# Optimization experiments

Hardware: AMD Instinct MI355X
Metric: run time of the kernel (lower is better)

## Reference

```python
import jax, jax.numpy as jnp
import numpy as np
from jax import lax

DN = ('NCHW', 'OIHW', 'NCHW')
NUM_HEADS = 6


def _conv1x1(x, w):
    return lax.conv_general_dilated(x, w, (1, 1), 'VALID', dimension_numbers=DN)


def _dwconv3x3(x, w):
    # depthwise 3x3, groups == channels, padding 1
    return lax.conv_general_dilated(x, w, (1, 1), ((1, 1), (1, 1)),
                                    dimension_numbers=DN,
                                    feature_group_count=w.shape[0])


def setup_inputs() -> dict:
    key = jax.random.key(0)
    ks = jax.random.split(key, 7)
    b, dim, h, w = 4, 192, 128, 128
    inp = {
        'x': jax.random.normal(ks[0], (b, dim, h, w), jnp.float32),
        'ref': jax.random.normal(ks[1], (b, dim, h, w), jnp.float32),
        'w_qkv': jax.random.normal(ks[2], (dim * 3, dim, 1, 1), jnp.float32) * 0.05,
        'w_dw': jax.random.normal(ks[3], (dim * 3, 1, 3, 3), jnp.float32) * 0.1,
        'w_proj': jax.random.normal(ks[4], (dim, dim, 1, 1), jnp.float32) * 0.05,
        'temperature': jnp.ones((NUM_HEADS, 1, 1), jnp.float32),
        'attn_w': 0.2 * jnp.ones((4,), jnp.float32),
    }
    return inp


def reference(x, ref, w_qkv, w_dw, w_proj, temperature, attn_w):
    b, c, h, w = x.shape
    heads = NUM_HEADS
    C = c // heads  # per-head channel dim
    hw = h * w

    qkv = _dwconv3x3(_conv1x1(x, w_qkv), w_dw)        # [b, 3c, h, w]
    ref_qkv = _dwconv3x3(_conv1x1(ref, w_qkv), w_dw)  # shared weights

    q_shared = qkv[:, :c]            # q from x
    k_shared = ref_qkv[:, c:2 * c]   # k from ref
    v_shared = ref_qkv[:, 2 * c:]    # v from ref

    def to_heads(t):  # [b, c, h, w] -> [b, head, C, hw]
        return t.reshape(b, heads, C, hw)

    q = to_heads(q_shared)
    k = to_heads(k_shared)
    v = to_heads(v_shared)

    # L2-normalize along token dim (last axis)
    q = q / jnp.maximum(jnp.linalg.norm(q, axis=-1, keepdims=True), 1e-12)
    k = k / jnp.maximum(jnp.linalg.norm(k, axis=-1, keepdims=True), 1e-12)

    # channel-wise attention: [b, head, C, C]
    attn = jnp.einsum('bhcn,bhdn->bhcd', q, k) * temperature

    ks_list = [int(C / 2), int(C * 2 / 3), int(C * 3 / 4), int(C * 4 / 5)]
    neg_inf = jnp.asarray(-jnp.inf, attn.dtype)

    out = 0.0
    for i, ki in enumerate(ks_list):
        vals = lax.top_k(attn, ki)[0]            # [b, head, C, ki]
        thr = vals[..., -1:]                     # k-th largest per row
        a = jnp.where(attn >= thr, attn, neg_inf)
        a = jax.nn.softmax(a, axis=-1)
        out = out + attn_w[i] * jnp.einsum('bhcd,bhdn->bhcn', a, v)

    out = out.reshape(b, c, h, w)
    return _conv1x1(out, w_proj)
```

## Files before the change

kernel.cpp:

```cpp
#include <hip/hip_runtime.h>
#include <cstdint>
#include <cstddef>

typedef unsigned short u16;
typedef unsigned int u32;
typedef __attribute__((ext_vector_type(2))) float f32x2;
typedef __attribute__((ext_vector_type(4))) float f32x4;
typedef __attribute__((ext_vector_type(8))) short short8;
typedef __attribute__((ext_vector_type(2))) u32 u32x2;
typedef __attribute__((ext_vector_type(4))) u32 u32x4;

#define DEV static __device__ __forceinline__
#define HW 16384

DEV u16 f2bf(float f) {
  u32 u = __float_as_uint(f);
  u = (u + 0x7fffu + ((u >> 16) & 1u)) >> 16;
  return (u16)u;
}
DEV float bf2f(u16 h) { return __uint_as_float(((u32)h) << 16); }

DEV u32 packsplit(float f) {
  u16 h = f2bf(f);
  u16 l = f2bf(f - bf2f(h));
  return (u32)h | ((u32)l << 16);
}
DEV void unpack8(const u32* w, short8& hi, short8& lo) {
  #pragma unroll
  for (int i = 0; i < 8; ++i) {
    hi[i] = (short)(u16)w[i];
    lo[i] = (short)(u16)(w[i] >> 16);
  }
}
DEV void mfma3(f32x4& acc, short8 ah, short8 al, short8 bh, short8 bl) {
  acc = __builtin_amdgcn_mfma_f32_16x16x32_bf16(ah, bh, acc, 0, 0, 0);
  acc = __builtin_amdgcn_mfma_f32_16x16x32_bf16(ah, bl, acc, 0, 0, 0);
  acc = __builtin_amdgcn_mfma_f32_16x16x32_bf16(al, bh, acc, 0, 0, 0);
}

__global__ __launch_bounds__(256) void ksplit(const float* __restrict__ in,
                                              u32* __restrict__ out, int n) {
  int i = blockIdx.x * 256 + threadIdx.x;
  if (i < n) out[i] = packsplit(in[i]);
}

template<int ABATCH, int BPACKED>
__global__ __launch_bounds__(512, 4) void gemm2(const u32* __restrict__ Asp,
                                                const u32* __restrict__ B,
                                                float* __restrict__ C) {
  __shared__ u32 As[192 * 34];
  __shared__ u32 Bs[64 * 34];
  const int t = threadIdx.x, lane = t & 63, wid = t >> 6;
  const int b = blockIdx.z, n0 = blockIdx.x * 64;
  const u32* Ab = ABATCH ? (Asp + (size_t)b * 192 * 192) : Asp;
  const u32* Bb = B + (size_t)b * 192 * (size_t)HW;
  float* Cb = C + (size_t)b * 192 * (size_t)HW;
  const int wr = wid >> 2, wc = wid & 3;
  const int g = lane >> 4, r16 = lane & 15;
  const int b_n = (t & 15) * 4, b_k = t >> 4;
  f32x4 acc[6] = {};

  u32x4 Breg, Bnext;
  u32x4 Areg[3];
  Breg = *(const u32x4*)&Bb[(size_t)b_k * HW + n0 + b_n];
  #pragma unroll
  for (int i = 0; i < 3; ++i) {
    int vi = t + i * 512;
    Areg[i] = *(const u32x4*)&Ab[(size_t)(vi >> 3) * 192 + ((vi & 7) << 2)];
  }
  #pragma unroll 1
  for (int p = 0; p < 6; ++p) {
    #pragma unroll
    for (int j = 0; j < 4; ++j)
      Bs[(b_n + j) * 34 + b_k] = BPACKED ? Breg[j] : packsplit(__uint_as_float(Breg[j]));
    #pragma unroll
    for (int i = 0; i < 3; ++i) {
      int vi = t + i * 512;
      int row = vi >> 3, kc = (vi & 7) << 2;
      u32x2 v0 = {Areg[i][0], Areg[i][1]};
      u32x2 v1 = {Areg[i][2], Areg[i][3]};
      *(u32x2*)&As[row * 34 + kc] = v0;
      *(u32x2*)&As[row * 34 + kc + 2] = v1;
    }
    if (p < 5)
      Bnext = *(const u32x4*)&Bb[(size_t)((p + 1) * 32 + b_k) * HW + n0 + b_n];
    __syncthreads();
    if (p < 5) {
      #pragma unroll
      for (int i = 0; i < 3; ++i) {
        int vi = t + i * 512;
        Areg[i] = *(const u32x4*)&Ab[(size_t)(vi >> 3) * 192 + (p + 1) * 32 + ((vi & 7) << 2)];
      }
    }
    u32 bw[8];
    {
      const u32* bp = &Bs[(wc * 16 + r16) * 34 + g * 8];
      *(u32x2*)&bw[0] = *(const u32x2*)&bp[0];
      *(u32x2*)&bw[2] = *(const u32x2*)&bp[2];
      *(u32x2*)&bw[4] = *(const u32x2*)&bp[4];
      *(u32x2*)&bw[6] = *(const u32x2*)&bp[6];
    }
    short8 bh, bl; unpack8(bw, bh, bl);
    #pragma unroll
    for (int mf = 0; mf < 6; ++mf) {
      u32 aw[8];
      const u32* ap = &As[(wr * 96 + mf * 16 + r16) * 34 + g * 8];
      *(u32x2*)&aw[0] = *(const u32x2*)&ap[0];
      *(u32x2*)&aw[2] = *(const u32x2*)&ap[2];
      *(u32x2*)&aw[4] = *(const u32x2*)&ap[4];
      *(u32x2*)&aw[6] = *(const u32x2*)&ap[6];
      short8 ah, al; unpack8(aw, ah, al);
      acc[mf] = __builtin_amdgcn_mfma_f32_16x16x32_bf16(ah, bh, acc[mf], 0, 0, 0);
      acc[mf] = __builtin_amdgcn_mfma_f32_16x16x32_bf16(ah, bl, acc[mf], 0, 0, 0);
      acc[mf] = __builtin_amdgcn_mfma_f32_16x16x32_bf16(al, bh, acc[mf], 0, 0, 0);
    }
    __syncthreads();
    Breg = Bnext;
  }
  #pragma unroll
  for (int mf = 0; mf < 6; ++mf)
    #pragma unroll
    for (int rr = 0; rr < 4; ++rr)
      Cb[(size_t)(wr * 96 + mf * 16 + g * 4 + rr) * HW + n0 + wc * 16 + r16] =
          acc[mf][rr];
}

template<int SSQ>
__global__ __launch_bounds__(512) void k2_dw(const float* __restrict__ Tin,
                                             const float* __restrict__ wdw, int wco,
                                             u32* __restrict__ O,
                                             float* __restrict__ ssq, int sspath) {
  const int rt = blockIdx.x, cg = blockIdx.y, b = blockIdx.z;
  const int t = threadIdx.x, lane = t & 63, w = t >> 6;
  __shared__ float In[8][10][132];
  for (int idx = t; idx < 10400; idx += 512) {
    int ch = idx / 1300, rem = idx % 1300;
    int r = rem / 130, ci = rem % 130;
    int gr = rt * 8 + r - 1, gc = ci - 1;
    float v = 0.f;
    if (gr >= 0 && gr < 128 && gc >= 0 && gc < 128)
      v = Tin[((size_t)b * 192 + cg * 8 + ch) * HW + gr * 128 + gc];
    In[ch][r][ci] = v;
  }
  float wv[9];
  #pragma unroll
  for (int j = 0; j < 9; ++j) wv[j] = wdw[(size_t)(wco + cg * 8 + w) * 9 + j];
  __syncthreads();
  float s = 0.f;
  u32* Op = O + ((size_t)b * 192 + cg * 8 + w) * HW + rt * 8 * 128 + 2 * lane;
  #pragma unroll
  for (int i = 0; i < 8; ++i) {
    float a0 = 0.f, a1 = 0.f;
    #pragma unroll
    for (int dr = 0; dr < 3; ++dr) {
      f32x2 u0 = *(const f32x2*)&In[w][i + dr][2 * lane];
      f32x2 u1 = *(const f32x2*)&In[w][i + dr][2 * lane + 2];
      a0 += wv[dr * 3] * u0[0] + wv[dr * 3 + 1] * u0[1] + wv[dr * 3 + 2] * u1[0];
      a1 += wv[dr * 3] * u0[1] + wv[dr * 3 + 1] * u1[0] + wv[dr * 3 + 2] * u1[1];
    }
    u32x2 o = {packsplit(a0), packsplit(a1)};
    *(u32x2*)&Op[(size_t)i * 128] = o;
    if (SSQ) s += a0 * a0 + a1 * a1;
  }
  if (SSQ) {
    #pragma unroll
    for (int off = 32; off; off >>= 1) s += __shfl_down(s, off);
    if (lane == 0) ssq[(((size_t)b * 2 + sspath) * 192 + cg * 8 + w) * 16 + rt] = s;
  }
}

__global__ __launch_bounds__(256) void k3_gram(const u32* __restrict__ q,
                                               const u32* __restrict__ k,
                                               float* __restrict__ gp) {
  const int ck = blockIdx.x, bh = blockIdx.y;
  const int b = bh / 6, h = bh % 6;
  const int t = threadIdx.x, lane = t & 63, wid = t >> 6;
  const int r16 = lane & 15, g = lane >> 4;
  const int chunk = ck * 4 + wid;
  const size_t rbase = ((size_t)b * 192 + h * 32 + r16) * HW;
  const u32* qp = q + rbase;
  const u32* kp = k + rbase;
  __shared__ float red[4][1024];
  f32x4 acc[2][2] = {};
  #pragma unroll 1
  for (int s = 0; s < 8; ++s) {
    int n = chunk * 256 + s * 32 + g * 8;
    u32 wq0[8], wq1[8], wk0[8], wk1[8];
    *(u32x4*)&wq0[0] = *(const u32x4*)&qp[n];
    *(u32x4*)&wq0[4] = *(const u32x4*)&qp[n + 4];
    *(u32x4*)&wq1[0] = *(const u32x4*)&qp[(size_t)16 * HW + n];
    *(u32x4*)&wq1[4] = *(const u32x4*)&qp[(size_t)16 * HW + n + 4];
    *(u32x4*)&wk0[0] = *(const u32x4*)&kp[n];
    *(u32x4*)&wk0[4] = *(const u32x4*)&kp[n + 4];
    *(u32x4*)&wk1[0] = *(const u32x4*)&kp[(size_t)16 * HW + n];
    *(u32x4*)&wk1[4] = *(const u32x4*)&kp[(size_t)16 * HW + n + 4];
    short8 a0h, a0l, a1h, a1l, b0h, b0l, b1h, b1l;
    unpack8(wq0, a0h, a0l);
    unpack8(wq1, a1h, a1l);
    unpack8(wk0, b0h, b0l);
    unpack8(wk1, b1h, b1l);
    mfma3(acc[0][0], a0h, a0l, b0h, b0l);
    mfma3(acc[0][1], a0h, a0l, b1h, b1l);
    mfma3(acc[1][0], a1h, a1l, b0h, b0l);
    mfma3(acc[1][1], a1h, a1l, b1h, b1l);
  }
  #pragma unroll
  for (int mf = 0; mf < 2; ++mf)
    #pragma unroll
    for (int nf = 0; nf < 2; ++nf)
      #pragma unroll
      for (int rr = 0; rr < 4; ++rr)
        red[wid][(mf * 16 + g * 4 + rr) * 32 + nf * 16 + r16] = acc[mf][nf][rr];
  __syncthreads();
  float* outp = gp + ((size_t)bh * 16 + ck) * 1024;
  #pragma unroll
  for (int e = t; e < 1024; e += 256)
    outp[e] = red[0][e] + red[1][e] + red[2][e] + red[3][e];
}

__global__ __launch_bounds__(256) void k4_comb(const float* __restrict__ gp,
                                               const float* __restrict__ ssq,
                                               const float* __restrict__ temp,
                                               const float* __restrict__ aw,
                                               const float* __restrict__ wproj,
                                               u32* __restrict__ mcp) {
  const int bh = blockIdx.x, b = bh / 6, h = bh % 6;
  const int t = threadIdx.x;
  __shared__ float Gs[1024];
  __shared__ float Acm[1024];
  __shared__ float nq[32], nk[32];
  {
    const float* p = gp + (size_t)bh * 16 * 1024 + 4 * t;
    f32x4 s = {};
    #pragma unroll
    for (int ch = 0; ch < 16; ++ch) {
      f32x4 v = *(const f32x4*)&p[(size_t)ch * 1024];
      s[0] += v[0]; s[1] += v[1]; s[2] += v[2]; s[3] += v[3];
    }
    *(f32x4*)&Gs[4 * t] = s;
  }
  if (t < 64) {
    int c = t & 31, pk = t >> 5;
    const float* sp = ssq + (((size_t)b * 2 + pk) * 192 + h * 32 + c) * 16;
    float s = 0.f;
    #pragma unroll
    for (int i = 0; i < 16; ++i) s += sp[i];
    float nr = fmaxf(sqrtf(s), 1e-12f);
    if (pk == 0) nq[c] = nr; else nk[c] = nr;
  }
  __syncthreads();
  const float T = temp[h];
  for (int e = t; e < 1024; e += 256) {
    int c = e >> 5, d = e & 31;
    Gs[e] = Gs[e] * T / (nq[c] * nk[d]);
  }
  __syncthreads();
  const float aw0 = aw[0], aw1 = aw[1], aw2 = aw[2], aw3 = aw[3];
  const int half = t >> 5, d = t & 31;
  for (int it = 0; it < 4; ++it) {
    const int c = it * 8 + half;
    const float v = Gs[c * 32 + d];
    int cnt = 0;
    #pragma unroll
    for (int dd = 0; dd < 32; ++dd) cnt += (Gs[c * 32 + dd] >= v) ? 1 : 0;
    float c0 = v;
    float c1 = (cnt >= 16) ? v : -3.0e38f;
    float c2 = (cnt >= 21) ? v : -3.0e38f;
    float c3 = (cnt >= 24) ? v : -3.0e38f;
    float c4 = (cnt >= 25) ? v : -3.0e38f;
    #pragma unroll
    for (int off = 16; off; off >>= 1) {
      c0 = fmaxf(c0, __shfl_xor(c0, off));
      c1 = fmaxf(c1, __shfl_xor(c1, off));
      c2 = fmaxf(c2, __shfl_xor(c2, off));
      c3 = fmaxf(c3, __shfl_xor(c3, off));
      c4 = fmaxf(c4, __shfl_xor(c4, off));
    }
    const float m = c0;
    const float ex = expf(v - m);
    float z1 = (v >= c1) ? ex : 0.f;
    float z2 = (v >= c2) ? ex : 0.f;
    float z3 = (v >= c3) ? ex : 0.f;
    float z4 = (v >= c4) ? ex : 0.f;
    #pragma unroll
    for (int off = 16; off; off >>= 1) {
      z1 += __shfl_xor(z1, off);
      z2 += __shfl_xor(z2, off);
      z3 += __shfl_xor(z3, off);
      z4 += __shfl_xor(z4, off);
    }
    float a = 0.f;
    a += (v >= c1) ? aw0 * ex / z1 : 0.f;
    a += (v >= c2) ? aw1 * ex / z2 : 0.f;
    a += (v >= c3) ? aw2 * ex / z3 : 0.f;
    a += (v >= c4) ? aw3 * ex / z4 : 0.f;
    Acm[c * 32 + d] = a;
  }
  __syncthreads();
  for (int idx = t; idx < 192 * 32; idx += 256) {
    int co = idx >> 5, dd = idx & 31;
    const float* wp = wproj + (size_t)co * 192 + h * 32;
    float s = 0.f;
    #pragma unroll
    for (int c = 0; c < 32; ++c) s += wp[c] * Acm[c * 32 + dd];
    mcp[((size_t)b * 192 + co) * 192 + h * 32 + dd] = packsplit(s);
  }
}

extern "C" void kernel_launch(void* const* d_in, const int* in_sizes, int n_in,
                              void* d_out, int out_size, void* d_ws, size_t ws_size,
                              hipStream_t stream) {
  const float* x     = (const float*)d_in[0];
  const float* ref   = (const float*)d_in[1];
  const float* wqkv  = (const float*)d_in[2];
  const float* wdw   = (const float*)d_in[3];
  const float* wproj = (const float*)d_in[4];
  const float* temp  = (const float*)d_in[5];
  const float* aw    = (const float*)d_in[6];
  float* out = (float*)d_out;
  char* ws = (char*)d_ws;

  const size_t S = (size_t)4 * 192 * HW * 4;
  float* tA  = (float*)(ws);
  float* tB  = (float*)(ws + S);
  u32*   qpk = (u32*)(ws + 2 * S);
  u32*   kpk = (u32*)(ws + 3 * S);
  float* gp  = (float*)(ws + 4 * S);
  float* ssq = (float*)(ws + 4 * S + 1572864);
  u32*   wsp = (u32*)(ws + 4 * S + 1572864 + 98304);
  u32*   mcp = (u32*)(ws + 4 * S + 1572864 + 98304 + 442368);
  u32*   vpk = (u32*)tB;

  ksplit<<<dim3(432), 256, 0, stream>>>(wqkv, wsp, 576 * 192);
  gemm2<0, 0><<<dim3(256, 1, 4), 512, 0, stream>>>(wsp, (const u32*)x, tA);
  k2_dw<1><<<dim3(16, 24, 4), 512, 0, stream>>>(tA, wdw, 0, qpk, ssq, 0);
  gemm2<0, 0><<<dim3(256, 1, 4), 512, 0, stream>>>(wsp + 192 * 192, (const u32*)ref, tB);
  k2_dw<1><<<dim3(16, 24, 4), 512, 0, stream>>>(tB, wdw, 192, kpk, ssq, 1);
  k3_gram<<<dim3(16, 24), 256, 0, stream>>>(qpk, kpk, gp);
  gemm2<0, 0><<<dim3(256, 1, 4), 512, 0, stream>>>(wsp + 384 * 192, (const u32*)ref, tA);
  k2_dw<0><<<dim3(16, 24, 4), 512, 0, stream>>>(tA, wdw, 384, vpk, nullptr, 2);
  k4_comb<<<dim3(24), 256, 0, stream>>>(gp, ssq, temp, aw, wproj, mcp);
  gemm2<1, 1><<<dim3(256, 1, 4), 512, 0, stream>>>(mcp, vpk, out);
}
```

Baseline: 240.9 us.

## Fuse K and V projection GEMMs into one pass and tune combine kernel

The gemm2 kernel is templated on the number of M fragments so that the K and V 1x1 projections of `ref` run as a single 384-row GEMM. This reads `ref` and splits it into bf16 hi/lo pairs once instead of twice. The depthwise kernel gets an input channel stride so it can consume the combined 384-channel buffer, and workspace buffers are re-aliased to fit. The combine kernel moves to 512 threads and stages the projection weights in shared memory. The trade-off is a larger LDS footprint and more accumulator registers per block in the fused GEMM, which can lower occupancy.

After: 233.0 us. 3.2% less time.

```diff
diff --git a/kernel.cpp b/kernel.cpp
--- a/kernel.cpp
+++ b/kernel.cpp
@@ -44,27 +44,28 @@
   if (i < n) out[i] = packsplit(in[i]);
 }
 
-template<int ABATCH, int BPACKED>
+template<int ABATCH, int BPACKED, int MFRAG>
 __global__ __launch_bounds__(512, 4) void gemm2(const u32* __restrict__ Asp,
                                                 const u32* __restrict__ B,
                                                 float* __restrict__ C) {
-  __shared__ u32 As[192 * 34];
+  constexpr int BM = MFRAG * 32;
+  __shared__ u32 As[BM * 34];
   __shared__ u32 Bs[64 * 34];
   const int t = threadIdx.x, lane = t & 63, wid = t >> 6;
   const int b = blockIdx.z, n0 = blockIdx.x * 64;
   const u32* Ab = ABATCH ? (Asp + (size_t)b * 192 * 192) : Asp;
   const u32* Bb = B + (size_t)b * 192 * (size_t)HW;
-  float* Cb = C + (size_t)b * 192 * (size_t)HW;
+  float* Cb = C + (size_t)b * BM * (size_t)HW;
   const int wr = wid >> 2, wc = wid & 3;
   const int g = lane >> 4, r16 = lane & 15;
   const int b_n = (t & 15) * 4, b_k = t >> 4;
-  f32x4 acc[6] = {};
+  f32x4 acc[MFRAG] = {};
 
   u32x4 Breg, Bnext;
-  u32x4 Areg[3];
+  u32x4 Areg[MFRAG / 2];
   Breg = *(const u32x4*)&Bb[(size_t)b_k * HW + n0 + b_n];
   #pragma unroll
-  for (int i = 0; i < 3; ++i) {
+  for (int i = 0; i < MFRAG / 2; ++i) {
     int vi = t + i * 512;
     Areg[i] = *(const u32x4*)&Ab[(size_t)(vi >> 3) * 192 + ((vi & 7) << 2)];
   }
@@ -74,7 +75,7 @@
     for (int j = 0; j < 4; ++j)
       Bs[(b_n + j) * 34 + b_k] = BPACKED ? Breg[j] : packsplit(__uint_as_float(Breg[j]));
     #pragma unroll
-    for (int i = 0; i < 3; ++i) {
+    for (int i = 0; i < MFRAG / 2; ++i) {
       int vi = t + i * 512;
       int row = vi >> 3, kc = (vi & 7) << 2;
       u32x2 v0 = {Areg[i][0], Areg[i][1]};
@@ -87,7 +88,7 @@
     __syncthreads();
     if (p < 5) {
       #pragma unroll
-      for (int i = 0; i < 3; ++i) {
+      for (int i = 0; i < MFRAG / 2; ++i) {
         int vi = t + i * 512;
         Areg[i] = *(const u32x4*)&Ab[(size_t)(vi >> 3) * 192 + (p + 1) * 32 + ((vi & 7) << 2)];
       }
@@ -102,9 +103,9 @@
     }
     short8 bh, bl; unpack8(bw, bh, bl);
     #pragma unroll
-    for (int mf = 0; mf < 6; ++mf) {
+    for (int mf = 0; mf < MFRAG; ++mf) {
       u32 aw[8];
-      const u32* ap = &As[(wr * 96 + mf * 16 + r16) * 34 + g * 8];
+      const u32* ap = &As[(wr * (MFRAG * 16) + mf * 16 + r16) * 34 + g * 8];
       *(u32x2*)&aw[0] = *(const u32x2*)&ap[0];
       *(u32x2*)&aw[2] = *(const u32x2*)&ap[2];
       *(u32x2*)&aw[4] = *(const u32x2*)&ap[4];
@@ -118,15 +119,15 @@
     Breg = Bnext;
   }
   #pragma unroll
-  for (int mf = 0; mf < 6; ++mf)
+  for (int mf = 0; mf < MFRAG; ++mf)
     #pragma unroll
     for (int rr = 0; rr < 4; ++rr)
-      Cb[(size_t)(wr * 96 + mf * 16 + g * 4 + rr) * HW + n0 + wc * 16 + r16] =
+      Cb[(size_t)(wr * (MFRAG * 16) + mf * 16 + g * 4 + rr) * HW + n0 + wc * 16 + r16] =
           acc[mf][rr];
 }
 
 template<int SSQ>
-__global__ __launch_bounds__(512) void k2_dw(const float* __restrict__ Tin,
+__global__ __launch_bounds__(512) void k2_dw(const float* __restrict__ Tin, int cstIn,
                                              const float* __restrict__ wdw, int wco,
                                              u32* __restrict__ O,
                                              float* __restrict__ ssq, int sspath) {
@@ -139,7 +140,7 @@
     int gr = rt * 8 + r - 1, gc = ci - 1;
     float v = 0.f;
     if (gr >= 0 && gr < 128 && gc >= 0 && gc < 128)
-      v = Tin[((size_t)b * 192 + cg * 8 + ch) * HW + gr * 128 + gc];
+      v = Tin[((size_t)b * cstIn + cg * 8 + ch) * HW + gr * 128 + gc];
     In[ch][r][ci] = v;
   }
   float wv[9];
@@ -218,7 +219,7 @@
     outp[e] = red[0][e] + red[1][e] + red[2][e] + red[3][e];
 }
 
-__global__ __launch_bounds__(256) void k4_comb(const float* __restrict__ gp,
+__global__ __launch_bounds__(512) void k4_comb(const float* __restrict__ gp,
                                                const float* __restrict__ ssq,
                                                const float* __restrict__ temp,
                                                const float* __restrict__ aw,
@@ -228,37 +229,53 @@
   const int t = threadIdx.x;
   __shared__ float Gs[1024];
   __shared__ float Acm[1024];
+  __shared__ float Wp[192 * 32];
   __shared__ float nq[32], nk[32];
+  #pragma unroll
+  for (int i = 0; i < 3; ++i) {
+    int idx = t + i * 512;
+    int row = idx >> 3, c4 = (idx & 7) << 2;
+    *(f32x4*)&Wp[row * 32 + c4] = *(const f32x4*)&wproj[(size_t)row * 192 + h * 32 + c4];
+  }
   {
-    const float* p = gp + (size_t)bh * 16 * 1024 + 4 * t;
-    f32x4 s = {};
+    const float* p = gp + (size_t)bh * 16 * 1024 + 2 * t;
+    f32x2 s = {};
     #pragma unroll
     for (int ch = 0; ch < 16; ++ch) {
-      f32x4 v = *(const f32x4*)&p[(size_t)ch * 1024];
-      s[0] += v[0]; s[1] += v[1]; s[2] += v[2]; s[3] += v[3];
-    }
-    *(f32x4*)&Gs[4 * t] = s;
+      f32x2 v = *(const f32x2*)&p[(size_t)ch * 1024];
+      s[0] += v[0]; s[1] += v[1];
+    }
+    *(f32x2*)&Gs[2 * t] = s;
   }
   if (t < 64) {
     int c = t & 31, pk = t >> 5;
     const float* sp = ssq + (((size_t)b * 2 + pk) * 192 + h * 32 + c) * 16;
-    float s = 0.f;
-    #pragma unroll
-    for (int i = 0; i < 16; ++i) s += sp[i];
-    float nr = fmaxf(sqrtf(s), 1e-12f);
+    f32x4 s4 = {};
+    #pragma unroll
+    for (int i = 0; i < 4; ++i) {
+      f32x4 v = *(const f32x4*)&sp[4 * i];
+      s4[0] += v[0]; s4[1] += v[1]; s4[2] += v[2]; s4[3] += v[3];
+    }
+    float nr = fmaxf(sqrtf(s4[0] + s4[1] + s4[2] + s4[3]), 1e-12f);
     if (pk == 0) nq[c] = nr; else nk[c] = nr;
   }
   __syncthreads();
   const float T = temp[h];
-  for (int e = t; e < 1024; e += 256) {
-    int c = e >> 5, d = e & 31;
-    Gs[e] = Gs[e] * T / (nq[c] * nk[d]);
+  {
+    int c = (2 * t) >> 5;
+    f32x2 v = *(const f32x2*)&Gs[2 * t];
+    float inq = T / nq[c];
+    v[0] = v[0] * inq / nk[(2 * t) & 31];
+    v[1] = v[1] * inq / nk[(2 * t + 1) & 31];
+    __syncthreads();
+    *(f32x2*)&Gs[2 * t] = v;
   }
   __syncthreads();
   const float aw0 = aw[0], aw1 = aw[1], aw2 = aw[2], aw3 = aw[3];
   const int half = t >> 5, d = t & 31;
-  for (int it = 0; it < 4; ++it) {
-    const int c = it * 8 + half;
+  #pragma unroll
+  for (int it = 0; it < 2; ++it) {
+    const int c = it * 16 + half;
     const float v = Gs[c * 32 + d];
     int cnt = 0;
     #pragma unroll
@@ -297,12 +314,13 @@
     Acm[c * 32 + d] = a;
   }
   __syncthreads();
-  for (int idx = t; idx < 192 * 32; idx += 256) {
+  #pragma unroll
+  for (int i = 0; i < 12; ++i) {
+    int idx = t + i * 512;
     int co = idx >> 5, dd = idx & 31;
-    const float* wp = wproj + (size_t)co * 192 + h * 32;
     float s = 0.f;
     #pragma unroll
-    for (int c = 0; c < 32; ++c) s += wp[c] * Acm[c * 32 + dd];
+    for (int c = 0; c < 32; ++c) s += Wp[co * 32 + c] * Acm[c * 32 + dd];
     mcp[((size_t)b * 192 + co) * 192 + h * 32 + dd] = packsplit(s);
   }
 }
@@ -322,23 +340,22 @@
 
   const size_t S = (size_t)4 * 192 * HW * 4;
   float* tA  = (float*)(ws);
-  float* tB  = (float*)(ws + S);
-  u32*   qpk = (u32*)(ws + 2 * S);
-  u32*   kpk = (u32*)(ws + 3 * S);
+  float* tKV = (float*)(ws + S);
+  u32*   qpk = (u32*)(ws + 3 * S);
   float* gp  = (float*)(ws + 4 * S);
   float* ssq = (float*)(ws + 4 * S + 1572864);
   u32*   wsp = (u32*)(ws + 4 * S + 1572864 + 98304);
   u32*   mcp = (u32*)(ws + 4 * S + 1572864 + 98304 + 442368);
-  u32*   vpk = (u32*)tB;
+  u32*   kpk = (u32*)tA;
+  u32*   vpk = qpk;
 
   ksplit<<<dim3(432), 256, 0, stream>>>(wqkv, wsp, 576 * 192);
-  gemm2<0, 0><<<dim3(256, 1, 4), 512, 0, stream>>>(wsp, (const u32*)x, tA);
-  k2_dw<1><<<dim3(16, 24, 4), 512, 0, stream>>>(tA, wdw, 0, qpk, ssq, 0);
-  gemm2<0, 0><<<dim3(256, 1, 4), 512, 0, stream>>>(wsp + 192 * 192, (const u32*)ref, tB);
-  k2_dw<1><<<dim3(16, 24, 4), 512, 0, stream>>>(tB, wdw, 192, kpk, ssq, 1);
+  gemm2<0, 0, 6><<<dim3(256, 1, 4), 512, 0, stream>>>(wsp, (const u32*)x, tA);
+  k2_dw<1><<<dim3(16, 24, 4), 512, 0, stream>>>(tA, 192, wdw, 0, qpk, ssq, 0);
+  gemm2<0, 0, 12><<<dim3(256, 1, 4), 512, 0, stream>>>(wsp + 192 * 192, (const u32*)ref, tKV);
+  k2_dw<1><<<dim3(16, 24, 4), 512, 0, stream>>>(tKV, 384, wdw, 192, kpk, ssq, 1);
   k3_gram<<<dim3(16, 24), 256, 0, stream>>>(qpk, kpk, gp);
-  gemm2<0, 0><<<dim3(256, 1, 4), 512, 0, stream>>>(wsp + 384 * 192, (const u32*)ref, tA);
-  k2_dw<0><<<dim3(16, 24, 4), 512, 0, stream>>>(tA, wdw, 384, vpk, nullptr, 2);
-  k4_comb<<<dim3(24), 256, 0, stream>>>(gp, ssq, temp, aw, wproj, mcp);
-  gemm2<1, 1><<<dim3(256, 1, 4), 512, 0, stream>>>(mcp, vpk, out);
-}
+  k2_dw<0><<<dim3(16, 24, 4), 512, 0, stream>>>(tKV + (size_t)192 * HW, 384, wdw, 384, vpk, nullptr, 2);
+  k4_comb<<<dim3(24), 512, 0, stream>>>(gp, ssq, temp, aw, wproj, mcp);
+  gemm2<1, 1, 6><<<dim3(256, 1, 4), 512, 0, stream>>>(mcp, vpk, out);
+}
```
